# Kernel optimization log

Measured on AMD Instinct MI355X. Metric: run time of the kernel, lower is better.

The kernel has to match this reference:

```python
import jax, jax.numpy as jnp
import numpy as np

B, S, D_IN, D_H = 4, 4096, 512, 64

def setup_inputs() -> dict:
    key = jax.random.key(0)
    ks = jax.random.split(key, 7)
    std = 1.0 / np.sqrt(D_IN)
    x = jax.random.normal(ks[0], (B, S, D_IN), dtype=jnp.float32)
    Wq = jax.random.uniform(ks[1], (D_IN, D_H), jnp.float32, -std, std)
    bq = jax.random.uniform(ks[2], (D_H,), jnp.float32, -std, std)
    Wk = jax.random.uniform(ks[3], (D_IN, D_H), jnp.float32, -std, std)
    bk = jax.random.uniform(ks[4], (D_H,), jnp.float32, -std, std)
    Wv = jax.random.uniform(ks[5], (D_IN, D_H), jnp.float32, -std, std)
    bv = jax.random.uniform(ks[6], (D_H,), jnp.float32, -std, std)
    return {"x": x, "Wq": Wq, "bq": bq, "Wk": Wk, "bk": bk, "Wv": Wv, "bv": bv}

def reference(x, Wq, bq, Wk, bk, Wv, bv):
    # q,k,v: [B, S, D_H]
    q = jnp.einsum('bsi,ih->bsh', x, Wq) + bq
    k = jnp.einsum('bsi,ih->bsh', x, Wk) + bk
    v = jnp.einsum('bsi,ih->bsh', x, Wv) + bv
    scale = 1.0 / jnp.sqrt(jnp.asarray(D_H, dtype=q.dtype))
    scores = jnp.einsum('bqh,bkh->bqk', q, k) * scale  # [B, S, S]
    att = jax.nn.softmax(scores, axis=-1)
    return jnp.einsum('bqk,bkh->bqh', att, v)
```

## Files before the change

kernel.cpp:

```cpp
#include <hip/hip_runtime.h>
#include <hip/hip_bf16.h>
#include <stdint.h>

#define LOG2E 1.4426950408889634f
#define SEQ 4096
#define DIN 512
#define DH 64
#define NSPLIT 8
#define QSCALE (0.125f * LOG2E)

typedef __attribute__((ext_vector_type(8))) short short8;
typedef __attribute__((ext_vector_type(16))) float f32x16;
typedef __attribute__((ext_vector_type(4))) float f32x4;

static __device__ __forceinline__ uint16_t f2bf(float f){
  uint32_t u = __float_as_uint(f);
  uint32_t r = u + 0x7fffu + ((u >> 16) & 1u);
  return (uint16_t)(r >> 16);
}

static __device__ __forceinline__ uint32_t cvt_pk_bf16(float lo, float hi){
  uint32_t d;
  asm("v_cvt_pk_bf16_f32 %0, %1, %2" : "=v"(d) : "v"(lo), "v"(hi));
  return d;
}

static __device__ __forceinline__ void perm32swap(uint32_t &a, uint32_t &b){
  asm("v_permlane32_swap_b32 %0, %1" : "+v"(a), "+v"(b));
}

static __device__ __forceinline__ float xadd32(float v){ return v + __shfl_xor(v, 32); }

static __device__ __forceinline__ void gload_lds16(const void* g, void* l){
  __builtin_amdgcn_global_load_lds(
      (const __attribute__((address_space(1))) unsigned int*)g,
      (__attribute__((address_space(3))) unsigned int*)l, 16, 0, 0);
}

__global__ void packw_kernel(const float* __restrict__ Wq, const float* __restrict__ Wk,
                             const float* __restrict__ Wv, uint4* __restrict__ Wp){
  int t0 = blockIdx.x * 256 + threadIdx.x;
  int lane = t0 & 63;
  int grp = t0 >> 6;
  int w3 = grp >> 6;
  int t  = (grp >> 2) & 15;
  int nc = grp & 3;
  const float* W = (w3 == 0) ? Wq : ((w3 == 1) ? Wk : Wv);
  int g = lane >> 4, cc = lane & 15;
  int k0 = t * 32 + g * 8;
  int n  = nc * 16 + cc;
  uint32_t o[4];
  #pragma unroll
  for (int p = 0; p < 4; ++p){
    float lo = W[(size_t)(k0 + 2*p    ) * DH + n];
    float hi = W[(size_t)(k0 + 2*p + 1) * DH + n];
    o[p] = cvt_pk_bf16(lo, hi);
  }
  Wp[(size_t)grp * 64 + lane] = make_uint4(o[0], o[1], o[2], o[3]);
}

__global__ __launch_bounds__(256) void proj_kernel(
    const float* __restrict__ x, const uint4* __restrict__ Wp,
    const float* __restrict__ bq, const float* __restrict__ bk, const float* __restrict__ bv,
    uint16_t* __restrict__ Qs, uint16_t* __restrict__ Kb, uint16_t* __restrict__ Vt)
{
  int tid = threadIdx.x, lane = tid & 63, wv = tid >> 6;
  int c = lane & 15, g = lane >> 4;
  int rowbase = blockIdx.x * 32;

  f32x4 acc[2][3];
  #pragma unroll
  for (int mt = 0; mt < 2; ++mt)
    #pragma unroll
    for (int j = 0; j < 3; ++j)
      #pragma unroll
      for (int r = 0; r < 4; ++r) acc[mt][j][r] = 0.f;

  const float* xr0 = x + (size_t)(rowbase + c) * DIN;
  const float* xr1 = x + (size_t)(rowbase + 16 + c) * DIN;

  #pragma unroll 2
  for (int t = 0; t < 16; ++t){
    short8 xa[2];
    #pragma unroll
    for (int mt = 0; mt < 2; ++mt){
      const float* p = (mt ? xr1 : xr0) + t * 32 + g * 8;
      float4 f0 = *(const float4*)(p);
      float4 f1 = *(const float4*)(p + 4);
      union { uint32_t u[4]; short8 s; } pk_;
      pk_.u[0] = cvt_pk_bf16(f0.x, f0.y);
      pk_.u[1] = cvt_pk_bf16(f0.z, f0.w);
      pk_.u[2] = cvt_pk_bf16(f1.x, f1.y);
      pk_.u[3] = cvt_pk_bf16(f1.z, f1.w);
      xa[mt] = pk_.s;
    }
    #pragma unroll
    for (int j = 0; j < 3; ++j){
      int i = wv * 3 + j;
      union { uint4 u; short8 s; } wf;
      wf.u = Wp[(size_t)((i >> 2) * 64 + t * 4 + (i & 3)) * 64 + lane];
      #pragma unroll
      for (int mt = 0; mt < 2; ++mt)
        acc[mt][j] = __builtin_amdgcn_mfma_f32_16x16x32_bf16(xa[mt], wf.s, acc[mt][j], 0, 0, 0);
    }
  }

  #pragma unroll
  for (int mt = 0; mt < 2; ++mt){
    int mb0 = rowbase + mt * 16 + 4 * g;
    #pragma unroll
    for (int j = 0; j < 3; ++j){
      int i = wv * 3 + j;
      int w3 = i >> 2, nc = i & 3, n = nc * 16 + c;
      const float* B = (w3 == 0) ? bq : ((w3 == 1) ? bk : bv);
      float bias = B[n];
      float v0 = acc[mt][j][0] + bias;
      float v1 = acc[mt][j][1] + bias;
      float v2 = acc[mt][j][2] + bias;
      float v3 = acc[mt][j][3] + bias;
      if (w3 == 0){
        Qs[(size_t)(mb0 + 0) * DH + n] = f2bf(v0 * QSCALE);
        Qs[(size_t)(mb0 + 1) * DH + n] = f2bf(v1 * QSCALE);
        Qs[(size_t)(mb0 + 2) * DH + n] = f2bf(v2 * QSCALE);
        Qs[(size_t)(mb0 + 3) * DH + n] = f2bf(v3 * QSCALE);
      } else if (w3 == 1){
        Kb[(size_t)(mb0 + 0) * DH + n] = f2bf(v0);
        Kb[(size_t)(mb0 + 1) * DH + n] = f2bf(v1);
        Kb[(size_t)(mb0 + 2) * DH + n] = f2bf(v2);
        Kb[(size_t)(mb0 + 3) * DH + n] = f2bf(v3);
      } else {
        int b = mb0 >> 12, mloc = mb0 & 4095;
        uint32_t lo = cvt_pk_bf16(v0, v1);
        uint32_t hi = cvt_pk_bf16(v2, v3);
        *(uint2*)(&Vt[((size_t)(b * DH + n)) * SEQ + mloc]) = make_uint2(lo, hi);
      }
    }
  }
}

__global__ __launch_bounds__(256, 3) void attn_kernel(
    const uint16_t* __restrict__ Qs, const uint16_t* __restrict__ Kb,
    const uint16_t* __restrict__ Vt, uint16_t* __restrict__ Pacc,
    float* __restrict__ Pl)
{
  __shared__ uint8_t lds[32768];
  const int tid = threadIdx.x, lane = tid & 63, wv = tid >> 6;
  const int bid = blockIdx.x;
  const int split = bid & 7, batch = (bid >> 3) & 3, qtile = bid >> 5;
  const int c = lane & 31, hi = lane >> 5;
  const int NT = SEQ / NSPLIT / 64;

  const int qrow = batch * SEQ + qtile * 128 + wv * 32 + c;

  short8 qf[4];
  {
    const uint16_t* qp = Qs + (size_t)qrow * DH;
    #pragma unroll
    for (int ks = 0; ks < 4; ++ks){
      union { uint4 u; short8 s; } v;
      v.u = *(const uint4*)(qp + ks * 16 + hi * 8);
      qf[ks] = v.s;
    }
  }

  int addr8[2][4];
  #pragma unroll
  for (int a = 0; a < 2; ++a)
    #pragma unroll
    for (int b = 0; b < 4; ++b)
      addr8[a][b] = (32 * a + c) * 128 + (((2 * b + hi) ^ (c & 7)) << 4);

  const int slotA = wv * 128 + lane, slotB = slotA + 64;
  const int keyA = slotA >> 3, keyB = slotB >> 3;
  const int dgA = (slotA & 7) ^ (keyA & 7), dgB = (slotB & 7) ^ (keyB & 7);
  const uint8_t* Kg = (const uint8_t*)Kb + ((size_t)(batch * SEQ + split * 512)) * (DH * 2);
  const uint8_t* KgA = Kg + keyA * 128 + dgA * 16;
  const uint8_t* KgB = Kg + keyB * 128 + dgB * 16;
  const uint8_t* Vg = (const uint8_t*)Vt + (size_t)batch * (DH * SEQ * 2) + split * 1024;
  const uint8_t* VgA = Vg + keyA * (SEQ * 2) + dgA * 16;
  const uint8_t* VgB = Vg + keyB * (SEQ * 2) + dgB * 16;

  f32x16 acc[2];
  #pragma unroll
  for (int d = 0; d < 2; ++d)
    #pragma unroll
    for (int r = 0; r < 16; ++r) acc[d][r] = 0.f;

  f32x16 ZERO;
  #pragma unroll
  for (int r = 0; r < 16; ++r) ZERO[r] = 0.f;
  asm volatile("" : "+v"(ZERO));

  float l0_ = 0.f, l1_ = 0.f, l2_ = 0.f, l3_ = 0.f;

  gload_lds16(KgA, lds + wv * 2048);
  gload_lds16(KgB, lds + wv * 2048 + 1024);
  gload_lds16(VgA, lds + 8192 + wv * 2048);
  gload_lds16(VgB, lds + 8192 + wv * 2048 + 1024);
  __syncthreads();

  #pragma unroll 1
  for (int t = 0; t < NT; ++t){
    const int OFF = (t & 1) << 14;
    const int NOFF = OFF ^ 16384;

    if (t < NT - 1){
      gload_lds16(KgA + (size_t)(t + 1) * 8192, lds + NOFF + wv * 2048);
      gload_lds16(KgB + (size_t)(t + 1) * 8192, lds + NOFF + wv * 2048 + 1024);
      gload_lds16(VgA + (size_t)(t + 1) * 128,  lds + NOFF + 8192 + wv * 2048);
      gload_lds16(VgB + (size_t)(t + 1) * 128,  lds + NOFF + 8192 + wv * 2048 + 1024);
    }

    f32x16 sa[2];
    __builtin_amdgcn_s_setprio(1);
    #pragma unroll
    for (int st = 0; st < 2; ++st){
      #pragma unroll
      for (int ks = 0; ks < 4; ++ks){
        short8 kf = *(const short8*)(lds + OFF + addr8[st][ks]);
        sa[st] = __builtin_amdgcn_mfma_f32_32x32x16_bf16(
            kf, qf[ks], (ks == 0) ? ZERO : sa[st], 0, 0, 0);
      }
    }
    __builtin_amdgcn_s_setprio(0);

    uint32_t pk[2][8];
    #pragma unroll
    for (int st = 0; st < 2; ++st){
      float pv[16];
      #pragma unroll
      for (int r = 0; r < 16; ++r) pv[r] = __builtin_amdgcn_exp2f(sa[st][r]);
      #pragma unroll
      for (int r = 0; r < 4; ++r){
        l0_ += pv[4 * r + 0];
        l1_ += pv[4 * r + 1];
        l2_ += pv[4 * r + 2];
        l3_ += pv[4 * r + 3];
      }
      #pragma unroll
      for (int p = 0; p < 8; ++p) pk[st][p] = cvt_pk_bf16(pv[2 * p], pv[2 * p + 1]);
    }

    short8 pf[4];
    #pragma unroll
    for (int kslab = 0; kslab < 4; ++kslab){
      int st = kslab >> 1, q4 = (kslab & 1) * 4;
      uint32_t w_[4];
      #pragma unroll
      for (int w1 = 0; w1 < 2; ++w1){
        uint32_t a = pk[st][q4 + w1];
        uint32_t b = pk[st][q4 + 2 + w1];
        perm32swap(a, b);
        w_[w1] = a; w_[2 + w1] = b;
      }
      union { uint32_t u[4]; short8 s; } u_;
      u_.u[0] = w_[0]; u_.u[1] = w_[1]; u_.u[2] = w_[2]; u_.u[3] = w_[3];
      pf[kslab] = u_.s;
    }

    __builtin_amdgcn_s_setprio(1);
    #pragma unroll
    for (int kslab = 0; kslab < 4; ++kslab){
      #pragma unroll
      for (int dst = 0; dst < 2; ++dst){
        short8 vf = *(const short8*)(lds + OFF + 8192 + addr8[dst][kslab]);
        acc[dst] = __builtin_amdgcn_mfma_f32_32x32x16_bf16(vf, pf[kslab], acc[dst], 0, 0, 0);
      }
    }
    __builtin_amdgcn_s_setprio(0);

    __syncthreads();
  }

  uint16_t* pa = Pacc + ((size_t)split * 16384 + qrow) * DH;
  #pragma unroll
  for (int dst = 0; dst < 2; ++dst)
    #pragma unroll
    for (int rq = 0; rq < 4; ++rq){
      uint32_t lo = cvt_pk_bf16(acc[dst][rq * 4 + 0], acc[dst][rq * 4 + 1]);
      uint32_t hi2 = cvt_pk_bf16(acc[dst][rq * 4 + 2], acc[dst][rq * 4 + 3]);
      *(uint2*)(pa + dst * 32 + rq * 8 + hi * 4) = make_uint2(lo, hi2);
    }
  float l_tot = xadd32((l0_ + l1_) + (l2_ + l3_));
  if (hi == 0) Pl[(size_t)split * 16384 + qrow] = l_tot;
}

__global__ __launch_bounds__(256) void combine_kernel(
    const uint16_t* __restrict__ Pacc, const float* __restrict__ Pl,
    float* __restrict__ out)
{
  int t = blockIdx.x * 256 + threadIdx.x;
  int q = t >> 2, part = t & 3;
  float l = 0.f;
  #pragma unroll
  for (int s = 0; s < NSPLIT; ++s) l += Pl[(size_t)s * 16384 + q];
  float inv = 1.0f / l;

  float o[16];
  #pragma unroll
  for (int i = 0; i < 16; ++i) o[i] = 0.f;
  #pragma unroll
  for (int s = 0; s < NSPLIT; ++s){
    const uint16_t* p = Pacc + ((size_t)s * 16384 + q) * DH + part * 16;
    #pragma unroll
    for (int h = 0; h < 2; ++h){
      uint4 v = *(const uint4*)(p + h * 8);
      const uint32_t* w = (const uint32_t*)&v;
      #pragma unroll
      for (int k = 0; k < 4; ++k){
        o[h * 8 + 2 * k + 0] += __uint_as_float((w[k] & 0xffffu) << 16);
        o[h * 8 + 2 * k + 1] += __uint_as_float((w[k] >> 16) << 16);
      }
    }
  }
  float* ob = out + (size_t)q * DH + part * 16;
  #pragma unroll
  for (int i = 0; i < 4; ++i){
    float4 v = make_float4(o[4*i] * inv, o[4*i+1] * inv, o[4*i+2] * inv, o[4*i+3] * inv);
    *(float4*)(ob + 4 * i) = v;
  }
}

extern "C" void kernel_launch(void* const* d_in, const int* in_sizes, int n_in,
                              void* d_out, int out_size, void* d_ws, size_t ws_size,
                              hipStream_t stream)
{
  (void)in_sizes; (void)n_in; (void)out_size; (void)ws_size;
  const float* x  = (const float*)d_in[0];
  const float* Wq = (const float*)d_in[1];
  const float* bq = (const float*)d_in[2];
  const float* Wk = (const float*)d_in[3];
  const float* bk = (const float*)d_in[4];
  const float* Wv = (const float*)d_in[5];
  const float* bv = (const float*)d_in[6];
  float* out = (float*)d_out;
  uint8_t* ws = (uint8_t*)d_ws;

  const size_t o_Wp = 0;
  const size_t o_Q  = 196608;
  const size_t o_K  = o_Q + 2097152;
  const size_t o_Vt = o_K + 2097152;
  const size_t o_Pa = o_Vt + 2097152;
  const size_t o_Pl = o_Pa + 16777216;

  packw_kernel<<<48, 256, 0, stream>>>(Wq, Wk, Wv, (uint4*)(ws + o_Wp));
  proj_kernel<<<512, 256, 0, stream>>>(x, (const uint4*)(ws + o_Wp), bq, bk, bv,
      (uint16_t*)(ws + o_Q), (uint16_t*)(ws + o_K), (uint16_t*)(ws + o_Vt));
  attn_kernel<<<1024, 256, 0, stream>>>((const uint16_t*)(ws + o_Q), (const uint16_t*)(ws + o_K),
      (const uint16_t*)(ws + o_Vt), (uint16_t*)(ws + o_Pa), (float*)(ws + o_Pl));
  combine_kernel<<<256, 256, 0, stream>>>((const uint16_t*)(ws + o_Pa), (const float*)(ws + o_Pl), out);
}
```

Measured before the change: 61.69 us.

## Triple-buffer K/V tiles in LDS with two-ahead prefetch and partial vmcnt waits

Measured after the change: 62.85 us. About the same (+1.9%).

```diff
diff --git a/kernel.cpp b/kernel.cpp
--- a/kernel.cpp
+++ b/kernel.cpp
@@ -143,7 +143,7 @@
     const uint16_t* __restrict__ Vt, uint16_t* __restrict__ Pacc,
     float* __restrict__ Pl)
 {
-  __shared__ uint8_t lds[32768];
+  __shared__ uint8_t lds[49152];
   const int tid = threadIdx.x, lane = tid & 63, wv = tid >> 6;
   const int bid = blockIdx.x;
   const int split = bid & 7, batch = (bid >> 3) & 3, qtile = bid >> 5;
@@ -197,19 +197,29 @@
   gload_lds16(KgB, lds + wv * 2048 + 1024);
   gload_lds16(VgA, lds + 8192 + wv * 2048);
   gload_lds16(VgB, lds + 8192 + wv * 2048 + 1024);
-  __syncthreads();
+  gload_lds16(KgA + 8192, lds + 16384 + wv * 2048);
+  gload_lds16(KgB + 8192, lds + 16384 + wv * 2048 + 1024);
+  gload_lds16(VgA + 128,  lds + 16384 + 8192 + wv * 2048);
+  gload_lds16(VgB + 128,  lds + 16384 + 8192 + wv * 2048 + 1024);
+  asm volatile("s_waitcnt vmcnt(4)" ::: "memory");
+  __builtin_amdgcn_s_barrier();
+  __builtin_amdgcn_sched_barrier(0);
+
+  int bc = 0;
+  int bs = 2;
 
   #pragma unroll 1
   for (int t = 0; t < NT; ++t){
-    const int OFF = (t & 1) << 14;
-    const int NOFF = OFF ^ 16384;
-
-    if (t < NT - 1){
-      gload_lds16(KgA + (size_t)(t + 1) * 8192, lds + NOFF + wv * 2048);
-      gload_lds16(KgB + (size_t)(t + 1) * 8192, lds + NOFF + wv * 2048 + 1024);
-      gload_lds16(VgA + (size_t)(t + 1) * 128,  lds + NOFF + 8192 + wv * 2048);
-      gload_lds16(VgB + (size_t)(t + 1) * 128,  lds + NOFF + 8192 + wv * 2048 + 1024);
-    }
+    const int off_c = bc << 14;
+
+    if (t < NT - 2){
+      const int off_s = bs << 14;
+      gload_lds16(KgA + (size_t)(t + 2) * 8192, lds + off_s + wv * 2048);
+      gload_lds16(KgB + (size_t)(t + 2) * 8192, lds + off_s + wv * 2048 + 1024);
+      gload_lds16(VgA + (size_t)(t + 2) * 128,  lds + off_s + 8192 + wv * 2048);
+      gload_lds16(VgB + (size_t)(t + 2) * 128,  lds + off_s + 8192 + wv * 2048 + 1024);
+    }
+    __builtin_amdgcn_sched_barrier(0);
 
     f32x16 sa[2];
     __builtin_amdgcn_s_setprio(1);
@@ -217,7 +227,7 @@
     for (int st = 0; st < 2; ++st){
       #pragma unroll
       for (int ks = 0; ks < 4; ++ks){
-        short8 kf = *(const short8*)(lds + OFF + addr8[st][ks]);
+        short8 kf = *(const short8*)(lds + off_c + addr8[st][ks]);
         sa[st] = __builtin_amdgcn_mfma_f32_32x32x16_bf16(
             kf, qf[ks], (ks == 0) ? ZERO : sa[st], 0, 0, 0);
       }
@@ -263,13 +273,23 @@
     for (int kslab = 0; kslab < 4; ++kslab){
       #pragma unroll
       for (int dst = 0; dst < 2; ++dst){
-        short8 vf = *(const short8*)(lds + OFF + 8192 + addr8[dst][kslab]);
+        short8 vf = *(const short8*)(lds + off_c + 8192 + addr8[dst][kslab]);
         acc[dst] = __builtin_amdgcn_mfma_f32_32x32x16_bf16(vf, pf[kslab], acc[dst], 0, 0, 0);
       }
     }
     __builtin_amdgcn_s_setprio(0);
 
-    __syncthreads();
+    if (t < NT - 2){
+      asm volatile("s_waitcnt vmcnt(4)" ::: "memory");
+      __builtin_amdgcn_s_barrier();
+    } else if (t < NT - 1){
+      asm volatile("s_waitcnt vmcnt(0)" ::: "memory");
+      __builtin_amdgcn_s_barrier();
+    }
+    __builtin_amdgcn_sched_barrier(0);
+
+    bc = (bc == 2) ? 0 : bc + 1;
+    bs = (bs == 2) ? 0 : bs + 1;
   }
 
   uint16_t* pa = Pacc + ((size_t)split * 16384 + qrow) * DH;
```

## Load K/V MFMA fragments directly from global memory instead of LDS staging

Applied to the files above, without the earlier changes.

Result: slower. 102.7 us (+66.4%).

```diff
diff --git a/kernel.cpp b/kernel.cpp
--- a/kernel.cpp
+++ b/kernel.cpp
@@ -30,12 +30,6 @@
 }
 
 static __device__ __forceinline__ float xadd32(float v){ return v + __shfl_xor(v, 32); }
-
-static __device__ __forceinline__ void gload_lds16(const void* g, void* l){
-  __builtin_amdgcn_global_load_lds(
-      (const __attribute__((address_space(1))) unsigned int*)g,
-      (__attribute__((address_space(3))) unsigned int*)l, 16, 0, 0);
-}
 
 __global__ void packw_kernel(const float* __restrict__ Wq, const float* __restrict__ Wk,
                              const float* __restrict__ Wv, uint4* __restrict__ Wp){
@@ -143,7 +137,6 @@
     const uint16_t* __restrict__ Vt, uint16_t* __restrict__ Pacc,
     float* __restrict__ Pl)
 {
-  __shared__ uint8_t lds[32768];
   const int tid = threadIdx.x, lane = tid & 63, wv = tid >> 6;
   const int bid = blockIdx.x;
   const int split = bid & 7, batch = (bid >> 3) & 3, qtile = bid >> 5;
@@ -163,22 +156,11 @@
     }
   }
 
-  int addr8[2][4];
-  #pragma unroll
-  for (int a = 0; a < 2; ++a)
-    #pragma unroll
-    for (int b = 0; b < 4; ++b)
-      addr8[a][b] = (32 * a + c) * 128 + (((2 * b + hi) ^ (c & 7)) << 4);
-
-  const int slotA = wv * 128 + lane, slotB = slotA + 64;
-  const int keyA = slotA >> 3, keyB = slotB >> 3;
-  const int dgA = (slotA & 7) ^ (keyA & 7), dgB = (slotB & 7) ^ (keyB & 7);
-  const uint8_t* Kg = (const uint8_t*)Kb + ((size_t)(batch * SEQ + split * 512)) * (DH * 2);
-  const uint8_t* KgA = Kg + keyA * 128 + dgA * 16;
-  const uint8_t* KgB = Kg + keyB * 128 + dgB * 16;
-  const uint8_t* Vg = (const uint8_t*)Vt + (size_t)batch * (DH * SEQ * 2) + split * 1024;
-  const uint8_t* VgA = Vg + keyA * (SEQ * 2) + dgA * 16;
-  const uint8_t* VgB = Vg + keyB * (SEQ * 2) + dgB * 16;
+  const uint8_t* Kgl = (const uint8_t*)Kb
+      + ((size_t)(batch * SEQ + split * 512 + c)) * 128 + hi * 16;
+  const uint8_t* Vgl0 = (const uint8_t*)Vt + (size_t)batch * (DH * SEQ * 2)
+      + (size_t)c * (SEQ * 2) + split * 1024 + hi * 16;
+  const uint8_t* Vgl1 = Vgl0 + (size_t)32 * (SEQ * 2);
 
   f32x16 acc[2];
   #pragma unroll
@@ -193,23 +175,11 @@
 
   float l0_ = 0.f, l1_ = 0.f, l2_ = 0.f, l3_ = 0.f;
 
-  gload_lds16(KgA, lds + wv * 2048);
-  gload_lds16(KgB, lds + wv * 2048 + 1024);
-  gload_lds16(VgA, lds + 8192 + wv * 2048);
-  gload_lds16(VgB, lds + 8192 + wv * 2048 + 1024);
-  __syncthreads();
-
   #pragma unroll 1
   for (int t = 0; t < NT; ++t){
-    const int OFF = (t & 1) << 14;
-    const int NOFF = OFF ^ 16384;
-
-    if (t < NT - 1){
-      gload_lds16(KgA + (size_t)(t + 1) * 8192, lds + NOFF + wv * 2048);
-      gload_lds16(KgB + (size_t)(t + 1) * 8192, lds + NOFF + wv * 2048 + 1024);
-      gload_lds16(VgA + (size_t)(t + 1) * 128,  lds + NOFF + 8192 + wv * 2048);
-      gload_lds16(VgB + (size_t)(t + 1) * 128,  lds + NOFF + 8192 + wv * 2048 + 1024);
-    }
+    const uint8_t* Kt = Kgl + (size_t)t * 8192;
+    const uint8_t* Vt0 = Vgl0 + (size_t)t * 128;
+    const uint8_t* Vt1 = Vgl1 + (size_t)t * 128;
 
     f32x16 sa[2];
     __builtin_amdgcn_s_setprio(1);
@@ -217,7 +187,7 @@
     for (int st = 0; st < 2; ++st){
       #pragma unroll
       for (int ks = 0; ks < 4; ++ks){
-        short8 kf = *(const short8*)(lds + OFF + addr8[st][ks]);
+        short8 kf = *(const short8*)(Kt + st * 4096 + ks * 32);
         sa[st] = __builtin_amdgcn_mfma_f32_32x32x16_bf16(
             kf, qf[ks], (ks == 0) ? ZERO : sa[st], 0, 0, 0);
       }
@@ -261,15 +231,12 @@
     __builtin_amdgcn_s_setprio(1);
     #pragma unroll
     for (int kslab = 0; kslab < 4; ++kslab){
-      #pragma unroll
-      for (int dst = 0; dst < 2; ++dst){
-        short8 vf = *(const short8*)(lds + OFF + 8192 + addr8[dst][kslab]);
-        acc[dst] = __builtin_amdgcn_mfma_f32_32x32x16_bf16(vf, pf[kslab], acc[dst], 0, 0, 0);
-      }
+      short8 vf0 = *(const short8*)(Vt0 + kslab * 32);
+      acc[0] = __builtin_amdgcn_mfma_f32_32x32x16_bf16(vf0, pf[kslab], acc[0], 0, 0, 0);
+      short8 vf1 = *(const short8*)(Vt1 + kslab * 32);
+      acc[1] = __builtin_amdgcn_mfma_f32_32x32x16_bf16(vf1, pf[kslab], acc[1], 0, 0, 0);
     }
     __builtin_amdgcn_s_setprio(0);
-
-    __syncthreads();
   }
 
   uint16_t* pa = Pacc + ((size_t)split * 16384 + qrow) * DH;
```
